# Performance work log

Measured on AMD Instinct MI355X. Metric: run time of the kernel, lower is better.

The kernel has to match this reference:

```python
import jax, jax.numpy as jnp
import numpy as np

B, S, D = 2, 2048, 2048
H, HD = 16, 128
WINDOW = 512
ROPE_BASE = 10000.0


def setup_inputs() -> dict:
    key = jax.random.key(0)
    k1, k2, k3 = jax.random.split(key, 3)
    x = jax.random.normal(k1, (B, S, D), dtype=jnp.float32)
    w_qkv = jax.random.normal(k2, (3 * D, D), dtype=jnp.float32) * (D ** -0.5)
    w_out = jax.random.normal(k3, (D, D), dtype=jnp.float32) * (D ** -0.5)
    return {"x": x, "w_qkv": w_qkv, "w_out": w_out}


def _rope_cos_sin(seq_len, head_dim, base, dtype):
    inv_freq = 1.0 / (base ** (jnp.arange(0, head_dim, 2, dtype=jnp.float32) / head_dim))
    pos = jnp.arange(seq_len, dtype=jnp.float32)
    freqs = pos[:, None] * inv_freq[None, :]            # (S, HD/2)
    emb = jnp.concatenate([freqs, freqs], axis=-1)       # (S, HD)
    return jnp.cos(emb).astype(dtype), jnp.sin(emb).astype(dtype)


def _rotate_half(x):
    x1, x2 = jnp.split(x, 2, axis=-1)
    return jnp.concatenate([-x2, x1], axis=-1)


def reference(x, w_qkv, w_out):
    Bx, Sx, Dx = x.shape
    # fused QKV projection (torch Linear: x @ W^T)
    qkv = jnp.einsum('bsd,ed->bse', x, w_qkv)
    q, k, v = jnp.split(qkv, 3, axis=-1)
    q = q.reshape(Bx, Sx, H, HD).transpose(0, 2, 1, 3)   # (B,H,S,HD)
    k = k.reshape(Bx, Sx, H, HD).transpose(0, 2, 1, 3)
    v = v.reshape(Bx, Sx, H, HD).transpose(0, 2, 1, 3)
    # RoPE with implicit position_ids = arange(S)
    cos, sin = _rope_cos_sin(Sx, HD, ROPE_BASE, x.dtype)  # (S, HD)
    q = q * cos[None, None] + _rotate_half(q) * sin[None, None]
    k = k * cos[None, None] + _rotate_half(k) * sin[None, None]
    # sliding-window attention: attend iff 0 <= i - j < WINDOW
    scale = 1.0 / jnp.sqrt(jnp.array(HD, dtype=x.dtype))
    scores = jnp.einsum('bhqd,bhkd->bhqk', q, k) * scale
    i = jnp.arange(Sx)[:, None]
    j = jnp.arange(Sx)[None, :]
    diff = i - j
    valid = (diff >= 0) & (diff < WINDOW)                # (S, S)
    scores = jnp.where(valid[None, None], scores, jnp.finfo(scores.dtype).min)
    attn = jax.nn.softmax(scores, axis=-1)
    out = jnp.einsum('bhqk,bhkd->bhqd', attn, v)
    out = out.transpose(0, 2, 1, 3).reshape(Bx, Sx, Dx)
    return jnp.einsum('bsd,ed->bse', out, w_out)
```

## Files before the change

kernel.cpp:

```cpp
#include <hip/hip_runtime.h>

#define S_LEN 2048
#define DIM 2048
#define NH 16
#define HD 128
#define WIN 512
#define QKVD (3 * DIM)

typedef unsigned short u16;
typedef unsigned int u32;
typedef __bf16 bf16x8 __attribute__((ext_vector_type(8)));
typedef float f32x4 __attribute__((ext_vector_type(4)));

__device__ __forceinline__ u16 f2bf(float f) {
  unsigned u = __builtin_bit_cast(unsigned, f);
  u += 0x7FFFu + ((u >> 16) & 1u);
  return (u16)(u >> 16);
}
__device__ __forceinline__ float bf2f(u16 b) {
  return __builtin_bit_cast(float, (unsigned)b << 16);
}
__device__ __forceinline__ void async16(const void* g, void* l) {
  __builtin_amdgcn_global_load_lds((__attribute__((address_space(1))) void*)g,
                                   (__attribute__((address_space(3))) void*)l,
                                   16, 0, 0);
}
#define WAITV(N) asm volatile("s_waitcnt vmcnt(" #N ")" ::: "memory")

__global__ __launch_bounds__(256) void cvt3tab_kernel(
    const float* __restrict__ a, u16* __restrict__ oa, int na,
    const float* __restrict__ b, u16* __restrict__ ob, int nb,
    const float* __restrict__ c, u16* __restrict__ oc, int nc,
    float* __restrict__ cosT, float* __restrict__ sinT, int nCvt) {
  if ((int)blockIdx.x >= nCvt) {
    int idx = ((int)blockIdx.x - nCvt) * 256 + threadIdx.x;
    int s = idx >> 6, j = idx & 63;
    double freq = exp((double)j * -0.14391156831212787);
    double ang = (double)s * freq;
    cosT[idx] = (float)cos(ang);
    sinT[idx] = (float)sin(ang);
    return;
  }
  int i = (blockIdx.x * 256 + threadIdx.x) * 4;
  const float* src;
  u16* dst;
  if (i < na) { src = a + i; dst = oa + i; }
  else if (i < na + nb) { src = b + (i - na); dst = ob + (i - na); }
  else if (i < na + nb + nc) { src = c + (i - na - nb); dst = oc + (i - na - nb); }
  else return;
  float4 v = *(const float4*)src;
  ushort4 o;
  o.x = f2bf(v.x); o.y = f2bf(v.y); o.z = f2bf(v.z); o.w = f2bf(v.w);
  *(ushort4*)dst = o;
}

template <int BN, typename TO>
__global__ __launch_bounds__(512, 2) void gemm8(const u16* __restrict__ A,
                                                const u16* __restrict__ B,
                                                TO* __restrict__ C,
                                                int M, int N, int K) {
  constexpr int ABY = 128 * 128;
  constexpr int BBY = BN * 128;
  constexpr int BLO = BN / 128;
  __shared__ __align__(16) char Al[2 * ABY];
  __shared__ __align__(16) char Bl[2 * BBY];

  const int tiles_n = N / BN;
  const int tiles_m = M >> 7;
  int m0, n0;
  if constexpr (BN == 384) {
    const int npx = tiles_n >> 3;
    const int xcd = (int)blockIdx.x & 7;
    const int idx = (int)blockIdx.x >> 3;
    m0 = (idx % tiles_m) << 7;
    n0 = (xcd * npx + idx / tiles_m) * BN;
  } else {
    const int nwg = gridDim.x;
    const int wg = ((int)blockIdx.x & 7) * (nwg >> 3) + ((int)blockIdx.x >> 3);
    m0 = (wg / tiles_n) << 7;
    n0 = (wg % tiles_n) * BN;
  }
  const int t = threadIdx.x;
  const int l = t & 63, w = t >> 6;
  const int wr = w >> 2, wc = w & 3;
  const int l16 = l & 15, lg = l >> 4;
  const u16* Asrc = A + (size_t)m0 * K;
  const u16* Bsrc = B + (size_t)n0 * K;

  auto stA = [&](int kcol, int half, int b) {
    int rih = t >> 3, ch = t & 7;
    int row = half * 64 + rih;
    async16(Asrc + (size_t)row * K + kcol + ((ch ^ (row & 7)) << 3),
            Al + b * ABY + row * 128 + ch * 16);
  };
  auto stB = [&](int kcol, int half, int b) {
#pragma unroll
    for (int j = 0; j < BLO; ++j) {
      int c = t + j * 512;
      int rih = c >> 3, ch = c & 7;
      int row = half * (BN / 2) + rih;
      async16(Bsrc + (size_t)row * K + kcol + ((ch ^ (row & 7)) << 3),
              Bl + b * BBY + row * 128 + ch * 16);
    }
  };

  f32x4 acc[4][2 * BLO] = {};
  bf16x8 af[2][2];
  bf16x8 bfr[2][BLO][2];

  auto rdA = [&](int b, int mh) {
#pragma unroll
    for (int m = 0; m < 2; ++m)
#pragma unroll
      for (int ks = 0; ks < 2; ++ks) {
        int row = wr * 64 + mh * 32 + m * 16 + l16;
        int ch = ks * 4 + lg;
        af[m][ks] = *(const bf16x8*)(Al + b * ABY + row * 128 + ((ch ^ (row & 7)) << 4));
      }
  };
  auto rdB = [&](int b, int nh) {
#pragma unroll
    for (int n = 0; n < BLO; ++n)
#pragma unroll
      for (int ks = 0; ks < 2; ++ks) {
        int row = wc * (BN / 4) + nh * (BN / 8) + n * 16 + l16;
        int ch = ks * 4 + lg;
        bfr[nh][n][ks] = *(const bf16x8*)(Bl + b * BBY + row * 128 + ((ch ^ (row & 7)) << 4));
      }
  };
  auto mm = [&](int mh, int nh) {
#pragma unroll
    for (int m = 0; m < 2; ++m)
#pragma unroll
      for (int n = 0; n < BLO; ++n)
#pragma unroll
        for (int ks = 0; ks < 2; ++ks)
          acc[mh * 2 + m][nh * BLO + n] = __builtin_amdgcn_mfma_f32_16x16x32_bf16(
              af[m][ks], bfr[nh][n][ks], acc[mh * 2 + m][nh * BLO + n], 0, 0, 0);
  };

  const int NT = K >> 6;
  stA(0, 0, 0); stB(0, 0, 0); stB(0, 1, 0); stA(0, 1, 0); stA(64, 0, 1);
  if constexpr (BN == 384) WAITV(5); else WAITV(4);
  __builtin_amdgcn_s_barrier();

  for (int kt = 0; kt < NT; ++kt) {
    const int b = kt & 1, nb = b ^ 1;
    const int k1 = ((kt + 1 < NT) ? kt + 1 : kt) << 6;
    const int k2 = ((kt + 2 < NT) ? kt + 2 : kt) << 6;
    rdA(b, 0); rdB(b, 0);
    stB(k1, 0, nb);
    __builtin_amdgcn_s_barrier();
    __builtin_amdgcn_s_setprio(1); mm(0, 0); __builtin_amdgcn_s_setprio(0);
    if constexpr (BN == 384) WAITV(5); else WAITV(4);
    __builtin_amdgcn_s_barrier();
    rdB(b, 1);
    stB(k1, 1, nb);
    __builtin_amdgcn_s_barrier();
    __builtin_amdgcn_s_setprio(1); mm(0, 1); __builtin_amdgcn_s_setprio(0);
    if constexpr (BN == 384) WAITV(7); else WAITV(5);
    __builtin_amdgcn_s_barrier();
    rdA(b, 1);
    stA(k1, 1, nb);
    __builtin_amdgcn_s_barrier();
    __builtin_amdgcn_s_setprio(1); mm(1, 0); __builtin_amdgcn_s_setprio(0);
    __builtin_amdgcn_s_barrier();
    stA(k2, 0, b);
    __builtin_amdgcn_s_barrier();
    __builtin_amdgcn_s_setprio(1); mm(1, 1); __builtin_amdgcn_s_setprio(0);
    if constexpr (BN == 384) WAITV(5); else WAITV(4);
    __builtin_amdgcn_s_barrier();
  }

  const int rb = m0 + wr * 64 + lg * 4;
  const int cb = n0 + wc * (BN / 4) + l16;
#pragma unroll
  for (int mi = 0; mi < 4; ++mi)
#pragma unroll
    for (int ni = 0; ni < 2 * BLO; ++ni)
#pragma unroll
      for (int r = 0; r < 4; ++r) {
        float v = acc[mi][ni][r];
        size_t idx2 = (size_t)(rb + mi * 16 + r) * N + cb + ni * 16;
        if constexpr (sizeof(TO) == 2) C[idx2] = f2bf(v);
        else C[idx2] = v;
      }
}

__global__ __launch_bounds__(256) void ropek_kernel(u16* __restrict__ qkv,
                                                    const float* __restrict__ cosT,
                                                    const float* __restrict__ sinT) {
  const int row = blockIdx.x * 2 + (threadIdx.x >> 7);
  const int s = row & (S_LEN - 1);
  const int slot = threadIdx.x & 127;
  const int h = slot >> 3;
  const int c = slot & 7;
  u16* p = qkv + (size_t)row * QKVD + DIM + h * HD + c * 8;
  const float* cp = cosT + (s << 6) + c * 8;
  const float* sp = sinT + (s << 6) + c * 8;
  const float4 c0 = *(const float4*)cp, c1 = *(const float4*)(cp + 4);
  const float4 s0 = *(const float4*)sp, s1 = *(const float4*)(sp + 4);
  float cs[8] = {c0.x, c0.y, c0.z, c0.w, c1.x, c1.y, c1.z, c1.w};
  float sn[8] = {s0.x, s0.y, s0.z, s0.w, s1.x, s1.y, s1.z, s1.w};
  uint4 lo = *(const uint4*)p;
  uint4 hi = *(const uint4*)(p + 64);
  unsigned lw[4] = {lo.x, lo.y, lo.z, lo.w};
  unsigned hw[4] = {hi.x, hi.y, hi.z, hi.w};
  unsigned ol[4], oh[4];
#pragma unroll
  for (int j = 0; j < 4; ++j) {
    float x1a = bf2f((u16)(lw[j] & 0xffffu)), x1b = bf2f((u16)(lw[j] >> 16));
    float x2a = bf2f((u16)(hw[j] & 0xffffu)), x2b = bf2f((u16)(hw[j] >> 16));
    float ca = cs[j * 2], cb = cs[j * 2 + 1];
    float sa = sn[j * 2], sb = sn[j * 2 + 1];
    ol[j] = (u32)f2bf(x1a * ca - x2a * sa) | ((u32)f2bf(x1b * cb - x2b * sb) << 16);
    oh[j] = (u32)f2bf(x2a * ca + x1a * sa) | ((u32)f2bf(x2b * cb + x1b * sb) << 16);
  }
  *(uint4*)p = (uint4){ol[0], ol[1], ol[2], ol[3]};
  *(uint4*)(p + 64) = (uint4){oh[0], oh[1], oh[2], oh[3]};
}

__global__ __launch_bounds__(512, 2) void attn_kernel(const u16* __restrict__ qkv,
                                                      u16* __restrict__ attnO,
                                                      const float* __restrict__ cosT,
                                                      const float* __restrict__ sinT) {
  const int nwg = gridDim.x;
  const int wg = ((int)blockIdx.x & 7) * (nwg >> 3) + ((int)blockIdx.x >> 3);
  const int qt = wg & 15;
  const int bh = wg >> 4;
  const int q0 = qt << 7;
  const int b = bh >> 4, h = bh & 15;
  const u16* Qp = qkv + (size_t)b * S_LEN * QKVD + h * HD;
  const u16* Kp = Qp + DIM;
  const u16* Vp = Qp + 2 * DIM;
  __shared__ __align__(16) char Ks[2][64 * 256];
  __shared__ __align__(16) u16 Vt[128][72];
  __shared__ __align__(16) u32 Ps[8][16 * 36];
  const int t = threadIdx.x;
  const int w = t >> 6, l = t & 63;
  const int l16 = l & 15, lg = l >> 4;
  const int q0w = q0 + w * 16;
  const bf16x8 ones = __builtin_bit_cast(bf16x8,
      (uint4){0x3F803F80u, 0x3F803F80u, 0x3F803F80u, 0x3F803F80u});
  bf16x8 qf[4];
  {
    const u16* qrow = Qp + (size_t)(q0w + l16) * QKVD;
#pragma unroll
    for (int ks = 0; ks < 4; ++ks) qf[ks] = *(const bf16x8*)(qrow + ks * 32 + lg * 8);
    const int srow = q0w + l16;
    const float* cbase = cosT + (srow << 6) + lg * 8;
    const float* sbase = sinT + (srow << 6) + lg * 8;
#pragma unroll
    for (int ks = 0; ks < 2; ++ks) {
      const float4 ca = *(const float4*)(cbase + ks * 32);
      const float4 cb2 = *(const float4*)(cbase + ks * 32 + 4);
      const float4 sa = *(const float4*)(sbase + ks * 32);
      const float4 sb2 = *(const float4*)(sbase + ks * 32 + 4);
      const float cs[8] = {ca.x, ca.y, ca.z, ca.w, cb2.x, cb2.y, cb2.z, cb2.w};
      const float sn[8] = {sa.x, sa.y, sa.z, sa.w, sb2.x, sb2.y, sb2.z, sb2.w};
      const uint4 lv = __builtin_bit_cast(uint4, qf[ks]);
      const uint4 hv = __builtin_bit_cast(uint4, qf[ks + 2]);
      const unsigned li[4] = {lv.x, lv.y, lv.z, lv.w};
      const unsigned hi2[4] = {hv.x, hv.y, hv.z, hv.w};
      unsigned lw[4], hw[4];
#pragma unroll
      for (int p2 = 0; p2 < 4; ++p2) {
        float f1a = bf2f((u16)(li[p2] & 0xffffu)), f1b = bf2f((u16)(li[p2] >> 16));
        float f2a = bf2f((u16)(hi2[p2] & 0xffffu)), f2b = bf2f((u16)(hi2[p2] >> 16));
        lw[p2] = (u32)f2bf(f1a * cs[p2 * 2] - f2a * sn[p2 * 2]) |
                 ((u32)f2bf(f1b * cs[p2 * 2 + 1] - f2b * sn[p2 * 2 + 1]) << 16);
        hw[p2] = (u32)f2bf(f2a * cs[p2 * 2] + f1a * sn[p2 * 2]) |
                 ((u32)f2bf(f2b * cs[p2 * 2 + 1] + f1b * sn[p2 * 2 + 1]) << 16);
      }
      qf[ks] = __builtin_bit_cast(bf16x8, (uint4){lw[0], lw[1], lw[2], lw[3]});
      qf[ks + 2] = __builtin_bit_cast(bf16x8, (uint4){hw[0], hw[1], hw[2], hw[3]});
    }
  }
  f32x4 oacc[8] = {};
  f32x4 ldacc = {};
  const int lo = max(0, (q0 - (WIN - 1)) >> 6);
  const int hi = (q0 + 127) >> 6;
  const int lo_w = max(0, (q0w - (WIN - 1)) >> 6);
  const int hi_w = (q0w + 15) >> 6;
  const float SC2 = 0.12751744654f;
  const int qi = q0w + l16;
  const int dc = t & 15, pr_ = t >> 4;

  auto loadV = [&](int kv0, uint4& va, uint4& vb) {
    va = *(const uint4*)(Vp + (size_t)(kv0 + pr_ * 2) * QKVD + dc * 8);
    vb = *(const uint4*)(Vp + (size_t)(kv0 + pr_ * 2 + 1) * QKVD + dc * 8);
  };
  auto issueK = [&](int kv0, int buf) {
#pragma unroll
    for (int i = 0; i < 2; ++i) {
      int c = t + (i << 9);
      int row = c >> 4, ch = c & 15;
      int sch = ch ^ (row & 7);
      async16(Kp + (size_t)(kv0 + row) * QKVD + sch * 8, Ks[buf] + c * 16);
    }
  };

  uint4 va, vb, va2, vb2;
  loadV(lo << 6, va, vb);
  __builtin_amdgcn_sched_barrier(0);
  issueK(lo << 6, 0);
  __builtin_amdgcn_sched_barrier(0);

  for (int kt = lo; kt <= hi; ++kt) {
    const int buf = (kt - lo) & 1;
    const int kv0 = kt << 6;
    const int ktn = (kt < hi) ? kt + 1 : hi;
    WAITV(2);
    __builtin_amdgcn_sched_barrier(0);
    __builtin_amdgcn_s_barrier();
    {
      const int kv = pr_ * 2, d0 = dc * 8;
      unsigned av[4] = {va.x, va.y, va.z, va.w};
      unsigned bv[4] = {vb.x, vb.y, vb.z, vb.w};
#pragma unroll
      for (int j = 0; j < 4; ++j) {
        *(unsigned*)&Vt[d0 + j * 2][kv] = (av[j] & 0xffffu) | (bv[j] << 16);
        *(unsigned*)&Vt[d0 + j * 2 + 1][kv] = (av[j] >> 16) | (bv[j] & 0xffff0000u);
      }
    }
    WAITV(0);
    asm volatile("s_waitcnt lgkmcnt(0)" ::: "memory");
    __builtin_amdgcn_sched_barrier(0);
    __builtin_amdgcn_s_barrier();
    loadV(ktn << 6, va2, vb2);
    __builtin_amdgcn_sched_barrier(0);
    issueK(ktn << 6, buf ^ 1);
    __builtin_amdgcn_sched_barrier(0);
    if (kt >= lo_w && kt <= hi_w) {
      u32* pbase = &Ps[w][0];
#pragma unroll
      for (int c4 = 0; c4 < 4; ++c4) {
        f32x4 sa = {};
#pragma unroll
        for (int ks = 0; ks < 4; ++ks) {
          const int krow = c4 * 16 + l16;
          const int ch = (ks * 4 + lg) ^ (krow & 7);
          bf16x8 kf = *(const bf16x8*)(Ks[buf] + krow * 256 + ch * 16);
          sa = __builtin_amdgcn_mfma_f32_16x16x32_bf16(kf, qf[ks], sa, 0, 0, 0);
        }
        const int kj_base = kv0 + c4 * 16 + lg * 4;
        float p[4];
#pragma unroll
        for (int r = 0; r < 4; ++r) {
          unsigned diff = (unsigned)(qi - (kj_base + r));
          float v = sa[r] * SC2;
          v = (diff < WIN) ? v : -1e30f;
          p[r] = __builtin_amdgcn_exp2f(v);
        }
        const u32 w0 = (u32)f2bf(p[0]) | ((u32)f2bf(p[1]) << 16);
        const u32 w1 = (u32)f2bf(p[2]) | ((u32)f2bf(p[3]) << 16);
        const int pw = l16 * 36 + c4 * 8 + lg * 2;
        pbase[pw] = w0;
        pbase[pw + 1] = w1;
      }
      asm volatile("s_waitcnt lgkmcnt(0)" ::: "memory");
      __builtin_amdgcn_sched_barrier(0);
#pragma unroll
      for (int ks = 0; ks < 2; ++ks) {
        uint4 pr2 = *(const uint4*)&Ps[w][l16 * 36 + ks * 16 + lg * 4];
        bf16x8 pf = __builtin_bit_cast(bf16x8, pr2);
#pragma unroll
        for (int dt = 0; dt < 8; ++dt) {
          bf16x8 vf = *(const bf16x8*)(&Vt[dt * 16 + l16][ks * 32 + lg * 8]);
          oacc[dt] = __builtin_amdgcn_mfma_f32_16x16x32_bf16(pf, vf, oacc[dt], 0, 0, 0);
        }
        ldacc = __builtin_amdgcn_mfma_f32_16x16x32_bf16(pf, ones, ldacc, 0, 0, 0);
      }
    }
    va = va2; vb = vb2;
  }
  const int qr = q0w + lg * 4;
  u16* orow = attnO + ((size_t)(b * S_LEN + qr) * DIM) + h * HD;
#pragma unroll
  for (int r = 0; r < 4; ++r) {
    float inv = 1.f / ldacc[r];
#pragma unroll
    for (int dt = 0; dt < 8; ++dt)
      orow[(size_t)r * DIM + dt * 16 + l16] = f2bf(oacc[dt][r] * inv);
  }
}

extern "C" void kernel_launch(void* const* d_in, const int* in_sizes, int n_in,
                              void* d_out, int out_size, void* d_ws, size_t ws_size,
                              hipStream_t stream) {
  const float* x = (const float*)d_in[0];
  const float* w_qkv = (const float*)d_in[1];
  const float* w_out = (const float*)d_in[2];
  float* out = (float*)d_out;

  char* ws = (char*)d_ws;
  size_t off = 0;
  auto alloc = [&](size_t bytes) {
    void* p = ws + off;
    off = (off + bytes + 255) & ~(size_t)255;
    return p;
  };
  const size_t rows = 2ull * S_LEN;
  u16* wqkvb = (u16*)alloc(3ull * DIM * DIM * 2);
  u16* woutb = (u16*)alloc((size_t)DIM * DIM * 2);
  u16* xb    = (u16*)alloc(rows * DIM * 2);
  u16* qkvb  = (u16*)alloc(rows * 3 * DIM * 2);
  float* cosT = (float*)alloc((size_t)S_LEN * 64 * 4);
  float* sinT = (float*)alloc((size_t)S_LEN * 64 * 4);

  const int na = 3 * DIM * DIM, nb = DIM * DIM, nc = (int)(rows * DIM);
  const int nCvt = (na + nb + nc) / 1024;
  cvt3tab_kernel<<<nCvt + (S_LEN * 64) / 256, 256, 0, stream>>>(
      w_qkv, wqkvb, na, w_out, woutb, nb, x, xb, nc, cosT, sinT, nCvt);
  gemm8<384, u16><<<(int)(rows / 128) * (QKVD / 384), 512, 0, stream>>>(
      xb, wqkvb, qkvb, (int)rows, QKVD, DIM);
  ropek_kernel<<<(int)(rows / 2), 256, 0, stream>>>(qkvb, cosT, sinT);
  u16* attnb = wqkvb;
  attn_kernel<<<2 * NH * (S_LEN / 128), 512, 0, stream>>>(qkvb, attnb, cosT, sinT);
  gemm8<256, float><<<(int)(rows / 128) * (DIM / 256), 512, 0, stream>>>(
      attnb, woutb, out, (int)rows, DIM, DIM);
}
```

Measured before the change: 228.7 us.

## Double attention query tile to 256 rows with two 16-row groups per wave

Each workgroup now handles 256 queries instead of 128, and each wave processes two 16-row query groups that share every loaded K fragment and V tile. This halves K/V global traffic and the V transpose work per query, and gives each wave more independent MFMAs. In exchange, register pressure roughly doubles, launch bounds drop to one block per CU, and the grid halves to 256 workgroups, which lowers occupancy and latency hiding.

Result: no change. 228.0 us (median of 2 runs) (-0.3%).

```diff
diff --git a/kernel.cpp b/kernel.cpp
--- a/kernel.cpp
+++ b/kernel.cpp
@@ -220,34 +220,35 @@
   *(uint4*)(p + 64) = (uint4){oh[0], oh[1], oh[2], oh[3]};
 }
 
-__global__ __launch_bounds__(512, 2) void attn_kernel(const u16* __restrict__ qkv,
+__global__ __launch_bounds__(512, 1) void attn_kernel(const u16* __restrict__ qkv,
                                                       u16* __restrict__ attnO,
                                                       const float* __restrict__ cosT,
                                                       const float* __restrict__ sinT) {
   const int nwg = gridDim.x;
   const int wg = ((int)blockIdx.x & 7) * (nwg >> 3) + ((int)blockIdx.x >> 3);
-  const int qt = wg & 15;
-  const int bh = wg >> 4;
-  const int q0 = qt << 7;
+  const int qt = wg & 7;
+  const int bh = wg >> 3;
+  const int q0 = qt << 8;
   const int b = bh >> 4, h = bh & 15;
   const u16* Qp = qkv + (size_t)b * S_LEN * QKVD + h * HD;
   const u16* Kp = Qp + DIM;
   const u16* Vp = Qp + 2 * DIM;
   __shared__ __align__(16) char Ks[2][64 * 256];
   __shared__ __align__(16) u16 Vt[128][72];
-  __shared__ __align__(16) u32 Ps[8][16 * 36];
+  __shared__ __align__(16) u32 Ps[8][2][16 * 36];
   const int t = threadIdx.x;
   const int w = t >> 6, l = t & 63;
   const int l16 = l & 15, lg = l >> 4;
-  const int q0w = q0 + w * 16;
+  const int q0w = q0 + w * 32;
   const bf16x8 ones = __builtin_bit_cast(bf16x8,
       (uint4){0x3F803F80u, 0x3F803F80u, 0x3F803F80u, 0x3F803F80u});
-  bf16x8 qf[4];
-  {
-    const u16* qrow = Qp + (size_t)(q0w + l16) * QKVD;
-#pragma unroll
-    for (int ks = 0; ks < 4; ++ks) qf[ks] = *(const bf16x8*)(qrow + ks * 32 + lg * 8);
-    const int srow = q0w + l16;
+  bf16x8 qf[2][4];
+#pragma unroll
+  for (int g = 0; g < 2; ++g) {
+    const int srow = q0w + g * 16 + l16;
+    const u16* qrow = Qp + (size_t)srow * QKVD;
+#pragma unroll
+    for (int ks = 0; ks < 4; ++ks) qf[g][ks] = *(const bf16x8*)(qrow + ks * 32 + lg * 8);
     const float* cbase = cosT + (srow << 6) + lg * 8;
     const float* sbase = sinT + (srow << 6) + lg * 8;
 #pragma unroll
@@ -258,8 +259,8 @@
       const float4 sb2 = *(const float4*)(sbase + ks * 32 + 4);
       const float cs[8] = {ca.x, ca.y, ca.z, ca.w, cb2.x, cb2.y, cb2.z, cb2.w};
       const float sn[8] = {sa.x, sa.y, sa.z, sa.w, sb2.x, sb2.y, sb2.z, sb2.w};
-      const uint4 lv = __builtin_bit_cast(uint4, qf[ks]);
-      const uint4 hv = __builtin_bit_cast(uint4, qf[ks + 2]);
+      const uint4 lv = __builtin_bit_cast(uint4, qf[g][ks]);
+      const uint4 hv = __builtin_bit_cast(uint4, qf[g][ks + 2]);
       const unsigned li[4] = {lv.x, lv.y, lv.z, lv.w};
       const unsigned hi2[4] = {hv.x, hv.y, hv.z, hv.w};
       unsigned lw[4], hw[4];
@@ -272,18 +273,17 @@
         hw[p2] = (u32)f2bf(f2a * cs[p2 * 2] + f1a * sn[p2 * 2]) |
                  ((u32)f2bf(f2b * cs[p2 * 2 + 1] + f1b * sn[p2 * 2 + 1]) << 16);
       }
-      qf[ks] = __builtin_bit_cast(bf16x8, (uint4){lw[0], lw[1], lw[2], lw[3]});
-      qf[ks + 2] = __builtin_bit_cast(bf16x8, (uint4){hw[0], hw[1], hw[2], hw[3]});
-    }
-  }
-  f32x4 oacc[8] = {};
-  f32x4 ldacc = {};
+      qf[g][ks] = __builtin_bit_cast(bf16x8, (uint4){lw[0], lw[1], lw[2], lw[3]});
+      qf[g][ks + 2] = __builtin_bit_cast(bf16x8, (uint4){hw[0], hw[1], hw[2], hw[3]});
+    }
+  }
+  f32x4 oacc[2][8] = {};
+  f32x4 ldacc[2] = {};
   const int lo = max(0, (q0 - (WIN - 1)) >> 6);
-  const int hi = (q0 + 127) >> 6;
+  const int hi = (q0 + 255) >> 6;
   const int lo_w = max(0, (q0w - (WIN - 1)) >> 6);
-  const int hi_w = (q0w + 15) >> 6;
+  const int hi_w = (q0w + 31) >> 6;
   const float SC2 = 0.12751744654f;
-  const int qi = q0w + l16;
   const int dc = t & 15, pr_ = t >> 4;
 
   auto loadV = [&](int kv0, uint4& va, uint4& vb) {
@@ -332,56 +332,68 @@
     issueK(ktn << 6, buf ^ 1);
     __builtin_amdgcn_sched_barrier(0);
     if (kt >= lo_w && kt <= hi_w) {
-      u32* pbase = &Ps[w][0];
 #pragma unroll
       for (int c4 = 0; c4 < 4; ++c4) {
-        f32x4 sa = {};
+        f32x4 sa0 = {}, sa1 = {};
 #pragma unroll
         for (int ks = 0; ks < 4; ++ks) {
           const int krow = c4 * 16 + l16;
           const int ch = (ks * 4 + lg) ^ (krow & 7);
           bf16x8 kf = *(const bf16x8*)(Ks[buf] + krow * 256 + ch * 16);
-          sa = __builtin_amdgcn_mfma_f32_16x16x32_bf16(kf, qf[ks], sa, 0, 0, 0);
+          sa0 = __builtin_amdgcn_mfma_f32_16x16x32_bf16(kf, qf[0][ks], sa0, 0, 0, 0);
+          sa1 = __builtin_amdgcn_mfma_f32_16x16x32_bf16(kf, qf[1][ks], sa1, 0, 0, 0);
         }
         const int kj_base = kv0 + c4 * 16 + lg * 4;
-        float p[4];
-#pragma unroll
-        for (int r = 0; r < 4; ++r) {
-          unsigned diff = (unsigned)(qi - (kj_base + r));
-          float v = sa[r] * SC2;
-          v = (diff < WIN) ? v : -1e30f;
-          p[r] = __builtin_amdgcn_exp2f(v);
+#pragma unroll
+        for (int g = 0; g < 2; ++g) {
+          const f32x4 sa = g ? sa1 : sa0;
+          const int qi = q0w + g * 16 + l16;
+          float p[4];
+#pragma unroll
+          for (int r = 0; r < 4; ++r) {
+            unsigned diff = (unsigned)(qi - (kj_base + r));
+            float v = sa[r] * SC2;
+            v = (diff < WIN) ? v : -1e30f;
+            p[r] = __builtin_amdgcn_exp2f(v);
+          }
+          const u32 w0 = (u32)f2bf(p[0]) | ((u32)f2bf(p[1]) << 16);
+          const u32 w1 = (u32)f2bf(p[2]) | ((u32)f2bf(p[3]) << 16);
+          const int pw = l16 * 36 + c4 * 8 + lg * 2;
+          Ps[w][g][pw] = w0;
+          Ps[w][g][pw + 1] = w1;
         }
-        const u32 w0 = (u32)f2bf(p[0]) | ((u32)f2bf(p[1]) << 16);
-        const u32 w1 = (u32)f2bf(p[2]) | ((u32)f2bf(p[3]) << 16);
-        const int pw = l16 * 36 + c4 * 8 + lg * 2;
-        pbase[pw] = w0;
-        pbase[pw + 1] = w1;
       }
       asm volatile("s_waitcnt lgkmcnt(0)" ::: "memory");
       __builtin_amdgcn_sched_barrier(0);
 #pragma unroll
       for (int ks = 0; ks < 2; ++ks) {
-        uint4 pr2 = *(const uint4*)&Ps[w][l16 * 36 + ks * 16 + lg * 4];
-        bf16x8 pf = __builtin_bit_cast(bf16x8, pr2);
+        uint4 p0 = *(const uint4*)&Ps[w][0][l16 * 36 + ks * 16 + lg * 4];
+        uint4 p1 = *(const uint4*)&Ps[w][1][l16 * 36 + ks * 16 + lg * 4];
+        bf16x8 pf0 = __builtin_bit_cast(bf16x8, p0);
+        bf16x8 pf1 = __builtin_bit_cast(bf16x8, p1);
 #pragma unroll
         for (int dt = 0; dt < 8; ++dt) {
           bf16x8 vf = *(const bf16x8*)(&Vt[dt * 16 + l16][ks * 32 + lg * 8]);
-          oacc[dt] = __builtin_amdgcn_mfma_f32_16x16x32_bf16(pf, vf, oacc[dt], 0, 0, 0);
+          oacc[0][dt] = __builtin_amdgcn_mfma_f32_16x16x32_bf16(pf0, vf, oacc[0][dt], 0, 0, 0);
+          oacc[1][dt] = __builtin_amdgcn_mfma_f32_16x16x32_bf16(pf1, vf, oacc[1][dt], 0, 0, 0);
         }
-        ldacc = __builtin_amdgcn_mfma_f32_16x16x32_bf16(pf, ones, ldacc, 0, 0, 0);
+        ldacc[0] = __builtin_amdgcn_mfma_f32_16x16x32_bf16(pf0, ones, ldacc[0], 0, 0, 0);
+        ldacc[1] = __builtin_amdgcn_mfma_f32_16x16x32_bf16(pf1, ones, ldacc[1], 0, 0, 0);
       }
     }
     va = va2; vb = vb2;
   }
-  const int qr = q0w + lg * 4;
-  u16* orow = attnO + ((size_t)(b * S_LEN + qr) * DIM) + h * HD;
-#pragma unroll
-  for (int r = 0; r < 4; ++r) {
-    float inv = 1.f / ldacc[r];
-#pragma unroll
-    for (int dt = 0; dt < 8; ++dt)
-      orow[(size_t)r * DIM + dt * 16 + l16] = f2bf(oacc[dt][r] * inv);
+#pragma unroll
+  for (int g = 0; g < 2; ++g) {
+    const int qr = q0w + g * 16 + lg * 4;
+    u16* orow = attnO + ((size_t)(b * S_LEN + qr) * DIM) + h * HD;
+#pragma unroll
+    for (int r = 0; r < 4; ++r) {
+      float inv = 1.f / ldacc[g][r];
+#pragma unroll
+      for (int dt = 0; dt < 8; ++dt)
+        orow[(size_t)r * DIM + dt * 16 + l16] = f2bf(oacc[g][dt][r] * inv);
+    }
   }
 }
 
@@ -416,7 +428,7 @@
       xb, wqkvb, qkvb, (int)rows, QKVD, DIM);
   ropek_kernel<<<(int)(rows / 2), 256, 0, stream>>>(qkvb, cosT, sinT);
   u16* attnb = wqkvb;
-  attn_kernel<<<2 * NH * (S_LEN / 128), 512, 0, stream>>>(qkvb, attnb, cosT, sinT);
+  attn_kernel<<<2 * NH * (S_LEN / 256), 512, 0, stream>>>(qkvb, attnb, cosT, sinT);
   gemm8<256, float><<<(int)(rows / 128) * (DIM / 256), 512, 0, stream>>>(
       attnb, woutb, out, (int)rows, DIM, DIM);
 }
```
